# Kernel optimization log

Hardware: AMD Instinct MI355X
Metric: run time of the kernel (lower is better)

## Reference

```python
import jax, jax.numpy as jnp
import numpy as np

N_DRUG, N_CELL, N_EDGES = 10000, 20000, 1280000
D_DRUG, D_CELL, BATCH = 384, 3504, 4096


def setup_inputs() -> dict:
    key = jax.random.key(0)
    ks = jax.random.split(key, 24)
    f32 = jnp.float32

    def lin(kw, kb, fan_in, fan_out, bias=True):
        s = 1.0 / np.sqrt(fan_in)
        W = jax.random.uniform(kw, (fan_in, fan_out), f32, -s, s)
        b = jax.random.uniform(kb, (fan_out,), f32, -s, s) if bias else None
        return W, b

    inp = {}
    inp['drug'] = jax.random.randint(ks[0], (BATCH,), 0, N_DRUG)
    inp['cell'] = jax.random.randint(ks[1], (BATCH,), 0, N_CELL)
    # stored node features / edges (constants in the torch module)
    inp['drug_x'] = jax.random.normal(ks[2], (N_DRUG, D_DRUG), f32)
    inp['cell_x'] = jax.random.normal(ks[3], (N_CELL, D_CELL), f32)
    inp['cell_edges'] = jax.random.randint(ks[4], (2, N_EDGES), 0, N_CELL)
    # drug_emb: Linear(384,128)
    inp['demb_W'], inp['demb_b'] = lin(ks[5], ks[6], D_DRUG, 128)
    # SAGEConv(3504,1024): lin_l (with bias) on aggregated, lin_r (no bias) on root
    inp['c1_lW'], inp['c1_lb'] = lin(ks[7], ks[8], D_CELL, 1024)
    inp['c1_rW'], _ = lin(ks[9], ks[9], D_CELL, 1024, bias=False)
    # SAGEConv(1024,256)
    inp['c2_lW'], inp['c2_lb'] = lin(ks[10], ks[11], 1024, 256)
    inp['c2_rW'], _ = lin(ks[12], ks[12], 1024, 256, bias=False)
    inp['reg_W1'], inp['reg_b1'] = lin(ks[13], ks[14], 384, 384)
    inp['reg_W2'], inp['reg_b2'] = lin(ks[15], ks[16], 384, 384)
    inp['reg_W3'], inp['reg_b3'] = lin(ks[17], ks[18], 384, 1)
    return inp


def _sage(x, src, dst, n, lW, lb, rW):
    # PyG SAGEConv, mean aggregation: lin_l(mean_{j in N(i)} x_j) + lin_r(x_i)
    deg = jax.ops.segment_sum(jnp.ones(src.shape[0], x.dtype), dst, num_segments=n)
    agg = jax.ops.segment_sum(x[src], dst, num_segments=n)  # [n, d_in]
    agg = agg / jnp.maximum(deg, 1.0)[:, None]
    return agg @ lW + lb + x @ rW


def reference(drug, cell, drug_x, cell_x, cell_edges,
              demb_W, demb_b, c1_lW, c1_lb, c1_rW, c2_lW, c2_lb, c2_rW,
              reg_W1, reg_b1, reg_W2, reg_b2, reg_W3, reg_b3):
    src, dst = cell_edges[0], cell_edges[1]
    n = cell_x.shape[0]
    # drug branch: Linear + ReLU (dropout = identity at inference)
    d = jax.nn.relu(drug_x @ demb_W + demb_b)                  # [N_drug, 128]
    # cell branch: two SAGEConv + ReLU
    c = jax.nn.relu(_sage(cell_x, src, dst, n, c1_lW, c1_lb, c1_rW))  # [N_cell, 1024]
    c = jax.nn.relu(_sage(c, src, dst, n, c2_lW, c2_lb, c2_rW))       # [N_cell, 256]
    # gather batch rows and concatenate -> [B, 384]
    x = jnp.concatenate([d[drug], c[cell]], axis=-1)
    x = jax.nn.elu(x @ reg_W1 + reg_b1)
    x = jax.nn.elu(x @ reg_W2 + reg_b2)
    return x @ reg_W3 + reg_b3                                 # [B, 1]
```

## Files before the change

kernel.cpp:

```cpp
#include <hip/hip_runtime.h>
#include <hip/hip_bf16.h>

typedef __bf16 bf16x8 __attribute__((ext_vector_type(8)));
typedef float f32x4 __attribute__((ext_vector_type(4)));
typedef unsigned short u16x8 __attribute__((ext_vector_type(8)));

#define N_DRUG   10000
#define N_CELL   20000
#define NEDGE    1280000
#define D_DRUG   384
#define D_CELL   3504
#define D_CELL_P 3520
#define BATCH    4096

typedef unsigned int u32_g __attribute__((address_space(1)));
typedef unsigned int u32_l __attribute__((address_space(3)));

__device__ __forceinline__ void gld_lds16(const void* g, void* l) {
  __builtin_amdgcn_global_load_lds((const u32_g*)g, (u32_l*)l, 16, 0, 0);
}

__device__ __forceinline__ ushort f2bf(float f) {
  union { float f; unsigned u; } v; v.f = f;
  unsigned r = v.u + 0x7fffu + ((v.u >> 16) & 1u);
  return (ushort)(r >> 16);
}
__device__ __forceinline__ float bf2f(ushort h) {
  union { unsigned u; float f; } v; v.u = ((unsigned)h) << 16;
  return v.f;
}

#define S_BARRIER() asm volatile("s_barrier" ::: "memory")
#define VMCNT6()    asm volatile("s_waitcnt vmcnt(6)" ::: "memory")
#define VMCNT0()    asm volatile("s_waitcnt vmcnt(0)" ::: "memory")


__global__ __launch_bounds__(256) void conv_x(const float* __restrict__ x,
                                              ushort* __restrict__ xb) {
  int idx = blockIdx.x * 256 + threadIdx.x;
  const int CH = D_CELL_P / 8;
  int r = idx / CH, c8 = (idx % CH) * 8;
  if (r >= N_CELL) return;
  ushort4 a, b;
  if (c8 < D_CELL) {
    const float* p = x + (size_t)r * D_CELL + c8;
    float4 v0 = *(const float4*)p;
    float4 v1 = *(const float4*)(p + 4);
    a = make_ushort4(f2bf(v0.x), f2bf(v0.y), f2bf(v0.z), f2bf(v0.w));
    b = make_ushort4(f2bf(v1.x), f2bf(v1.y), f2bf(v1.z), f2bf(v1.w));
  } else {
    a = make_ushort4(0,0,0,0); b = make_ushort4(0,0,0,0);
  }
  ushort* q = xb + (size_t)r * D_CELL_P + c8;
  *(ushort4*)q = a; *(ushort4*)(q + 4) = b;
}

__global__ __launch_bounds__(256) void conv_drug(const float* __restrict__ dx,
                                                 const int* __restrict__ drug,
                                                 ushort* __restrict__ adb) {
  int idx = blockIdx.x * 256 + threadIdx.x;
  int r = idx / 48, c8 = (idx % 48) * 8;
  int g = drug[r];
  const float* p = dx + (size_t)g * D_DRUG + c8;
  float4 v0 = *(const float4*)p, v1 = *(const float4*)(p + 4);
  ushort4 a = make_ushort4(f2bf(v0.x), f2bf(v0.y), f2bf(v0.z), f2bf(v0.w));
  ushort4 b = make_ushort4(f2bf(v1.x), f2bf(v1.y), f2bf(v1.z), f2bf(v1.w));
  ushort* q = adb + (size_t)r * D_DRUG + c8;
  *(ushort4*)q = a; *(ushort4*)(q + 4) = b;
}

__global__ __launch_bounds__(256) void conv_wt(const float* __restrict__ L,
                                               const float* __restrict__ R,
                                               int nL, int N, int Kin, int Kp,
                                               ushort* __restrict__ out) {
  __shared__ float tile[32][33];
  int k0 = blockIdx.x * 32, n0 = blockIdx.y * 32;
  int t = threadIdx.x;
  int tn = t & 31, tk = t >> 5;
  #pragma unroll
  for (int p = 0; p < 4; ++p) {
    int k = k0 + tk + p * 8, n = n0 + tn;
    float v = 0.f;
    if (k < Kin) v = (n < nL) ? L[(size_t)k * nL + n] : R[(size_t)k * (N - nL) + (n - nL)];
    tile[tk + p * 8][tn] = v;
  }
  __syncthreads();
  int wk = t & 31, wn = t >> 5;
  #pragma unroll
  for (int p = 0; p < 4; ++p) {
    int n = n0 + wn + p * 8, k = k0 + wk;
    out[(size_t)n * Kp + k] = f2bf(tile[wk][wn + p * 8]);
  }
}


__global__ void deg_kernel(const int* __restrict__ dst, int* __restrict__ deg, int n) {
  for (int e = blockIdx.x * blockDim.x + threadIdx.x; e < n; e += gridDim.x * blockDim.x)
    atomicAdd(&deg[dst[e]], 1);
}

__global__ __launch_bounds__(1024) void scan_kernel(const int* __restrict__ deg,
                                                    int* __restrict__ rowptr,
                                                    int* __restrict__ cursor, int n) {
  __shared__ int wsum[16];
  __shared__ int carry_s;
  int t = threadIdx.x, wave = t >> 6, lane = t & 63;
  if (t == 0) carry_s = 0;
  __syncthreads();
  for (int base = 0; base < n; base += 1024) {
    int x = (base + t < n) ? deg[base + t] : 0;
    int v = x;
    #pragma unroll
    for (int off = 1; off < 64; off <<= 1) {
      int u = __shfl_up(v, off, 64);
      if (lane >= off) v += u;
    }
    if (lane == 63) wsum[wave] = v;
    __syncthreads();
    if (wave == 0 && lane < 16) {
      int w = wsum[lane];
      #pragma unroll
      for (int off = 1; off < 16; off <<= 1) {
        int u = __shfl_up(w, off, 64);
        if (lane >= off) w += u;
      }
      wsum[lane] = w;
    }
    __syncthreads();
    int wpre = (wave == 0) ? 0 : wsum[wave - 1];
    int incl = v + wpre;
    int carry = carry_s;
    if (base + t < n) { int ex = carry + incl - x; rowptr[base + t] = ex; cursor[base + t] = ex; }
    __syncthreads();
    if (t == 1023) carry_s = carry + incl;
    __syncthreads();
  }
  if (t == 0) rowptr[n] = carry_s;
}

__global__ void bucket_kernel(const int* __restrict__ src, const int* __restrict__ dst,
                              int* __restrict__ cursor, int* __restrict__ srcs, int n) {
  for (int e = blockIdx.x * blockDim.x + threadIdx.x; e < n; e += gridDim.x * blockDim.x) {
    int p = atomicAdd(&cursor[dst[e]], 1);
    srcs[p] = src[e];
  }
}

__global__ void mark_kernel(const int* __restrict__ cell, int* __restrict__ mark) {
  int b = blockIdx.x * 256 + threadIdx.x;
  if (b < BATCH) mark[cell[b]] = 1;
}

__global__ __launch_bounds__(512, 2) void gemm8p(const ushort* __restrict__ A,
                                                 const ushort* __restrict__ Bt,
                                                 float* __restrict__ outF,
                                                 ushort* __restrict__ outB,
                                                 int M) {
  constexpr int K = D_CELL_P;
  constexpr int NK = K / 64;
  __shared__ ushort lds[2][2][32][512];

  const int t = threadIdx.x;
  const int wid = t >> 6, lane = t & 63;
  const int wr = wid >> 2, wc = wid & 3;
  const int brow = blockIdx.y * 256, bcol = blockIdx.x * 256;
  const int fr = lane & 15, kgi = lane >> 4;
  const int slot8 = (fr * 4 + (kgi ^ ((fr >> 1) & 3))) * 8;
  const int srow = lane >> 2;
  const int gsw = ((lane & 3) ^ ((lane >> 3) & 3)) * 8;

  f32x4 acc[8][4];
  #pragma unroll
  for (int m = 0; m < 8; ++m)
    #pragma unroll
    for (int n = 0; n < 4; ++n) acc[m][n] = f32x4{0.f, 0.f, 0.f, 0.f};

  bf16x8 af[4][2], bfg[4][2];

  auto stage = [&](int b, int h, int kt) {
    const ushort* base = (h < 2) ? A : Bt;
    const int rb = (h < 2) ? brow : bcol;
    const int half = h & 1, ab = h >> 1;
    const int k0 = kt * 64;
    #pragma unroll
    for (int j = 0; j < 2; ++j) {
      int c = j * 8 + wid;
      int r16 = half * 8 + (c >> 1), kc = c & 1;
      int row = rb + r16 * 16 + srow;
      if (h < 2) row = row < M ? row : M - 1;
      gld_lds16(base + (size_t)row * K + k0 + kc * 32 + gsw,
                &lds[b][ab][half * 16 + c][0]);
    }
  };

  stage(0, 0, 0); stage(0, 2, 0); stage(0, 3, 0); stage(0, 1, 0);
  stage(1, 0, 1); stage(1, 2, 1); stage(1, 3, 1);
  VMCNT6();
  S_BARRIER();

  for (int kt = 0; kt < NK; ++kt) {
    const int b = kt & 1, nb = b ^ 1;
    const bool dr = (kt >= NK - 2);

    #pragma unroll
    for (int m = 0; m < 4; ++m) {
      af[m][0] = *(const bf16x8*)&lds[b][0][(2 * m + wr) * 2 + 0][slot8];
      af[m][1] = *(const bf16x8*)&lds[b][0][(2 * m + wr) * 2 + 1][slot8];
    }
    #pragma unroll
    for (int n = 0; n < 2; ++n) {
      bfg[n][0] = *(const bf16x8*)&lds[b][1][(4 * n + wc) * 2 + 0][slot8];
      bfg[n][1] = *(const bf16x8*)&lds[b][1][(4 * n + wc) * 2 + 1][slot8];
    }
    if (kt + 1 < NK) stage(nb, 1, kt + 1);
    S_BARRIER();
    __builtin_amdgcn_s_setprio(1);
    #pragma unroll
    for (int m = 0; m < 4; ++m)
      #pragma unroll
      for (int n = 0; n < 2; ++n) {
        acc[m][n] = __builtin_amdgcn_mfma_f32_16x16x32_bf16(af[m][0], bfg[n][0], acc[m][n], 0, 0, 0);
        acc[m][n] = __builtin_amdgcn_mfma_f32_16x16x32_bf16(af[m][1], bfg[n][1], acc[m][n], 0, 0, 0);
      }
    __builtin_amdgcn_s_setprio(0);
    S_BARRIER();

    #pragma unroll
    for (int n = 2; n < 4; ++n) {
      bfg[n][0] = *(const bf16x8*)&lds[b][1][(4 * n + wc) * 2 + 0][slot8];
      bfg[n][1] = *(const bf16x8*)&lds[b][1][(4 * n + wc) * 2 + 1][slot8];
    }
    if (kt + 2 < NK) stage(b, 0, kt + 2);
    S_BARRIER();
    __builtin_amdgcn_s_setprio(1);
    #pragma unroll
    for (int m = 0; m < 4; ++m)
      #pragma unroll
      for (int n = 2; n < 4; ++n) {
        acc[m][n] = __builtin_amdgcn_mfma_f32_16x16x32_bf16(af[m][0], bfg[n][0], acc[m][n], 0, 0, 0);
        acc[m][n] = __builtin_amdgcn_mfma_f32_16x16x32_bf16(af[m][1], bfg[n][1], acc[m][n], 0, 0, 0);
      }
    __builtin_amdgcn_s_setprio(0);
    S_BARRIER();

    #pragma unroll
    for (int m = 0; m < 4; ++m) {
      af[m][0] = *(const bf16x8*)&lds[b][0][(2 * (m + 4) + wr) * 2 + 0][slot8];
      af[m][1] = *(const bf16x8*)&lds[b][0][(2 * (m + 4) + wr) * 2 + 1][slot8];
    }
    if (kt + 2 < NK) stage(b, 2, kt + 2);
    S_BARRIER();
    __builtin_amdgcn_s_setprio(1);
    #pragma unroll
    for (int m = 0; m < 4; ++m)
      #pragma unroll
      for (int n = 0; n < 2; ++n) {
        acc[m + 4][n] = __builtin_amdgcn_mfma_f32_16x16x32_bf16(af[m][0], bfg[n][0], acc[m + 4][n], 0, 0, 0);
        acc[m + 4][n] = __builtin_amdgcn_mfma_f32_16x16x32_bf16(af[m][1], bfg[n][1], acc[m + 4][n], 0, 0, 0);
      }
    __builtin_amdgcn_s_setprio(0);
    S_BARRIER();

    if (kt + 2 < NK) stage(b, 3, kt + 2);
    S_BARRIER();
    __builtin_amdgcn_s_setprio(1);
    #pragma unroll
    for (int m = 0; m < 4; ++m)
      #pragma unroll
      for (int n = 2; n < 4; ++n) {
        acc[m + 4][n] = __builtin_amdgcn_mfma_f32_16x16x32_bf16(af[m][0], bfg[n][0], acc[m + 4][n], 0, 0, 0);
        acc[m + 4][n] = __builtin_amdgcn_mfma_f32_16x16x32_bf16(af[m][1], bfg[n][1], acc[m + 4][n], 0, 0, 0);
      }
    __builtin_amdgcn_s_setprio(0);
    if (dr) { VMCNT0(); } else { VMCNT6(); }
    S_BARRIER();
  }

  #pragma unroll
  for (int m = 0; m < 8; ++m)
    #pragma unroll
    for (int n = 0; n < 4; ++n)
      #pragma unroll
      for (int j = 0; j < 4; ++j) {
        int row = brow + (2 * m + wr) * 16 + kgi * 4 + j;
        int col = bcol + (4 * n + wc) * 16 + fr;
        if (row < M) {
          float v = acc[m][n][j];
          if (col < 1024) outB[(size_t)row * 1024 + col] = f2bf(v);
          else            outF[(size_t)row * 1024 + (col - 1024)] = v;
        }
      }
}

template <int EPI>
__global__ __launch_bounds__(256) void gemm_bt(const ushort* __restrict__ A,
                                               const ushort* __restrict__ Bt,
                                               float* __restrict__ outF,
                                               ushort* __restrict__ outB,
                                               const float* __restrict__ bias,
                                               int M, int N, int K, int ldc) {
  __shared__ ushort ldsA[128 * 32];
  __shared__ ushort ldsB[128 * 32];
  const int t = threadIdx.x;
  const int wave = t >> 6, lane = t & 63;
  const int brow = blockIdx.y * 128;
  const int bcol = blockIdx.x * 128;
  const int wr = wave >> 1, wc = wave & 1;

  f32x4 acc[4][4];
  #pragma unroll
  for (int m = 0; m < 4; ++m)
    #pragma unroll
    for (int n = 0; n < 4; ++n) acc[m][n] = f32x4{0.f, 0.f, 0.f, 0.f};

  const int srow = lane >> 2;
  const int gsw  = ((lane & 3) ^ ((lane >> 3) & 3)) * 8;
  const int nk = K >> 5;

  const int fr = lane & 15;
  const int kgi = lane >> 4;
  const int slot = (fr * 4 + (kgi ^ ((fr >> 1) & 3))) * 8;

  for (int kt = 0; kt < nk; ++kt) {
    const int k0 = kt * 32;
    #pragma unroll
    for (int i = 0; i < 2; ++i) {
      int c = i * 4 + wave;
      int arow = brow + c * 16 + srow;
      arow = arow < M ? arow : M - 1;
      gld_lds16(A + (size_t)arow * K + k0 + gsw, ldsA + c * 512);
      int brB = bcol + c * 16 + srow;
      gld_lds16(Bt + (size_t)brB * K + k0 + gsw, ldsB + c * 512);
    }
    __syncthreads();
    bf16x8 af[4], bf[4];
    #pragma unroll
    for (int m = 0; m < 4; ++m) af[m] = *(const bf16x8*)(ldsA + (wr * 4 + m) * 512 + slot);
    #pragma unroll
    for (int n = 0; n < 4; ++n) bf[n] = *(const bf16x8*)(ldsB + (wc * 4 + n) * 512 + slot);
    #pragma unroll
    for (int m = 0; m < 4; ++m)
      #pragma unroll
      for (int n = 0; n < 4; ++n)
        acc[m][n] = __builtin_amdgcn_mfma_f32_16x16x32_bf16(af[m], bf[n], acc[m][n], 0, 0, 0);
    __syncthreads();
  }

  const int fq = lane >> 4;
  #pragma unroll
  for (int m = 0; m < 4; ++m) {
    #pragma unroll
    for (int n = 0; n < 4; ++n) {
      #pragma unroll
      for (int j = 0; j < 4; ++j) {
        int row = brow + wr * 64 + m * 16 + fq * 4 + j;
        int col = bcol + wc * 64 + n * 16 + fr;
        if (row < M) {
          float v = acc[m][n][j];
          if constexpr (EPI == 0) {
            outF[(size_t)row * ldc + col] = v;
          } else if constexpr (EPI == 2) {
            v += bias[col];
            v = fmaxf(v, 0.f);
            outB[(size_t)row * ldc + col] = f2bf(v);
          } else {
            v += bias[col];
            v = v > 0.f ? v : expm1f(v);
            outB[(size_t)row * ldc + col] = f2bf(v);
          }
        }
      }
    }
  }
}


__global__ __launch_bounds__(256) void agg1_c1(const ushort* __restrict__ Ylb,
                                               const float* __restrict__ Yr,
                                               const float* __restrict__ lb,
                                               const int* __restrict__ rowptr,
                                               const int* __restrict__ srcs,
                                               ushort* __restrict__ c1b) {
  const int b = blockIdx.x, t = threadIdx.x;
  const int s = b & 7;
  const int i = (b >> 3) * 4 + (t >> 6);
  const int lane = t & 63;
  const int eg = lane >> 4, c16 = lane & 15;
  const int s0 = rowptr[i], s1 = rowptr[i + 1];
  const ushort* base = Ylb + s * 128 + c16 * 8;

  float a[8] = {0.f, 0.f, 0.f, 0.f, 0.f, 0.f, 0.f, 0.f};
  int e = s0 + eg;
  for (; e + 4 < s1; e += 8) {
    int srcA = srcs[e], srcB = srcs[e + 4];
    u16x8 vA = *(const u16x8*)(base + (size_t)srcA * 1024);
    u16x8 vB = *(const u16x8*)(base + (size_t)srcB * 1024);
    #pragma unroll
    for (int k = 0; k < 8; ++k) a[k] += bf2f(vA[k]) + bf2f(vB[k]);
  }
  for (; e < s1; e += 4) {
    int src = srcs[e];
    u16x8 v = *(const u16x8*)(base + (size_t)src * 1024);
    #pragma unroll
    for (int k = 0; k < 8; ++k) a[k] += bf2f(v[k]);
  }
  #pragma unroll
  for (int k = 0; k < 8; ++k) {
    a[k] += __shfl_xor(a[k], 16, 64);
    a[k] += __shfl_xor(a[k], 32, 64);
  }
  if (eg == 0) {
    float inv = 1.0f / fmaxf((float)(s1 - s0), 1.0f);
    size_t off = (size_t)i * 1024 + s * 128 + c16 * 8;
    float4 y0 = *(const float4*)(Yr + off);
    float4 y1 = *(const float4*)(Yr + off + 4);
    float yr[8] = {y0.x, y0.y, y0.z, y0.w, y1.x, y1.y, y1.z, y1.w};
    u16x8 o;
    #pragma unroll
    for (int k = 0; k < 8; ++k) {
      float v = a[k] * inv + lb[s * 128 + c16 * 8 + k] + yr[k];
      o[k] = f2bf(fmaxf(v, 0.f));
    }
    *(u16x8*)(c1b + off) = o;
  }
}

__global__ __launch_bounds__(256) void agg2_c2(const float* __restrict__ Z,
                                               const float* __restrict__ lb,
                                               const int* __restrict__ rowptr,
                                               const int* __restrict__ srcs,
                                               const int* __restrict__ mark,
                                               ushort* __restrict__ c2v) {
  int i = blockIdx.x;
  if (!mark[i]) return;
  __shared__ int sl[256];
  int t = threadIdx.x;
  int s0 = rowptr[i], s1 = rowptr[i + 1];
  float a = 0.f;
  for (int base = s0; base < s1; base += 256) {
    int m = s1 - base; if (m > 256) m = 256;
    if (t < m) sl[t] = srcs[base + t];
    __syncthreads();
    int e = 0;
    for (; e + 4 <= m; e += 4) {
      float zA = Z[(size_t)sl[e] * 512 + t];
      float zB = Z[(size_t)sl[e + 1] * 512 + t];
      float zC = Z[(size_t)sl[e + 2] * 512 + t];
      float zD = Z[(size_t)sl[e + 3] * 512 + t];
      a += zA + zB + zC + zD;
    }
    for (; e < m; ++e) a += Z[(size_t)sl[e] * 512 + t];
    __syncthreads();
  }
  float inv = 1.0f / fmaxf((float)(s1 - s0), 1.0f);
  float v = a * inv + lb[t] + Z[(size_t)i * 512 + 256 + t];
  c2v[(size_t)i * 256 + t] = f2bf(fmaxf(v, 0.f));
}

__global__ __launch_bounds__(256) void xcat2(const ushort* __restrict__ c2v,
                                             const int* __restrict__ cell,
                                             ushort* __restrict__ xcat) {
  int idx = blockIdx.x * 256 + threadIdx.x;
  int b = idx >> 6, q = idx & 63;
  ushort4 v = *(const ushort4*)(c2v + (size_t)cell[b] * 256 + q * 4);
  *(ushort4*)(xcat + (size_t)b * 384 + 128 + q * 4) = v;
}

__global__ __launch_bounds__(256) void final_k(const ushort* __restrict__ h2,
                                               const float* __restrict__ W3,
                                               const float* __restrict__ b3,
                                               float* __restrict__ out) {
  int row = blockIdx.x * 4 + (threadIdx.x >> 6);
  int lane = threadIdx.x & 63;
  const ushort* p = h2 + (size_t)row * 384;
  float s = 0.f;
  #pragma unroll
  for (int k = lane; k < 384; k += 64) s += bf2f(p[k]) * W3[k];
  #pragma unroll
  for (int off = 32; off; off >>= 1) s += __shfl_xor(s, off, 64);
  if (lane == 0) out[row] = s + b3[0];
}


extern "C" void kernel_launch(void* const* d_in, const int* in_sizes, int n_in,
                              void* d_out, int out_size, void* d_ws, size_t ws_size,
                              hipStream_t stream) {
  (void)in_sizes; (void)n_in; (void)out_size; (void)ws_size;
  const int*   drug   = (const int*)  d_in[0];
  const int*   cell   = (const int*)  d_in[1];
  const float* drug_x = (const float*)d_in[2];
  const float* cell_x = (const float*)d_in[3];
  const int*   edges  = (const int*)  d_in[4];
  const float* demb_W = (const float*)d_in[5];
  const float* demb_b = (const float*)d_in[6];
  const float* c1_lW  = (const float*)d_in[7];
  const float* c1_lb  = (const float*)d_in[8];
  const float* c1_rW  = (const float*)d_in[9];
  const float* c2_lW  = (const float*)d_in[10];
  const float* c2_lb  = (const float*)d_in[11];
  const float* c2_rW  = (const float*)d_in[12];
  const float* reg_W1 = (const float*)d_in[13];
  const float* reg_b1 = (const float*)d_in[14];
  const float* reg_W2 = (const float*)d_in[15];
  const float* reg_b2 = (const float*)d_in[16];
  const float* reg_W3 = (const float*)d_in[17];
  const float* reg_b3 = (const float*)d_in[18];
  float* out = (float*)d_out;

  char* ws = (char*)d_ws;
  size_t off = 0;
  auto alloc = [&](size_t b) { size_t o = off; off += (b + 255) & ~(size_t)255; return o; };
  size_t oXB  = alloc((size_t)N_CELL * D_CELL_P * 2);
  size_t oW1T = alloc((size_t)2048 * D_CELL_P * 2);
  size_t oYLB = alloc((size_t)N_CELL * 1024 * 2);
  size_t oYR  = alloc((size_t)N_CELL * 1024 * 4);
  size_t oW2T = alloc((size_t)512 * 1024 * 2);
  size_t oSRC = alloc((size_t)NEDGE * 4);
  size_t oDEG = alloc((size_t)N_CELL * 4);
  size_t oRPT = alloc((size_t)(N_CELL + 1) * 4);
  size_t oCUR = alloc((size_t)N_CELL * 4);
  size_t oMRK = alloc((size_t)N_CELL * 4);
  size_t oADB = alloc((size_t)BATCH * D_DRUG * 2);
  size_t oWDT = alloc((size_t)128 * 384 * 2);
  size_t oXC  = alloc((size_t)BATCH * 384 * 2);
  size_t oW1R = alloc((size_t)384 * 384 * 2);
  size_t oW2R = alloc((size_t)384 * 384 * 2);
  size_t oH1  = alloc((size_t)BATCH * 384 * 2);
  size_t oH2  = alloc((size_t)BATCH * 384 * 2);

  ushort* Xb   = (ushort*)(ws + oXB);
  ushort* c1b  = (ushort*)(ws + oXB);
  float*  Z    = (float*) (ws + oXB + 40960000);
  ushort* c2v  = (ushort*)(ws + oXB + 81920000);
  ushort* W1t  = (ushort*)(ws + oW1T);
  ushort* Ylb  = (ushort*)(ws + oYLB);
  float*  Yr   = (float*) (ws + oYR);
  ushort* W2t  = (ushort*)(ws + oW2T);
  int*    srcs = (int*)   (ws + oSRC);
  int*    deg  = (int*)   (ws + oDEG);
  int*    rpt  = (int*)   (ws + oRPT);
  int*    cur  = (int*)   (ws + oCUR);
  int*    mrk  = (int*)   (ws + oMRK);
  ushort* Adb  = (ushort*)(ws + oADB);
  ushort* Wdt  = (ushort*)(ws + oWDT);
  ushort* xcat = (ushort*)(ws + oXC);
  ushort* W1rt = (ushort*)(ws + oW1R);
  ushort* W2rt = (ushort*)(ws + oW2R);
  ushort* h1   = (ushort*)(ws + oH1);
  ushort* h2   = (ushort*)(ws + oH2);

  const int* esrc = edges;
  const int* edst = edges + NEDGE;

  hipMemsetAsync(deg, 0, (size_t)N_CELL * 4, stream);
  hipMemsetAsync(mrk, 0, (size_t)N_CELL * 4, stream);

  deg_kernel<<<2048, 256, 0, stream>>>(edst, deg, NEDGE);
  scan_kernel<<<1, 1024, 0, stream>>>(deg, rpt, cur, N_CELL);
  bucket_kernel<<<2048, 256, 0, stream>>>(esrc, edst, cur, srcs, NEDGE);
  mark_kernel<<<BATCH / 256, 256, 0, stream>>>(cell, mrk);

  conv_x<<<(N_CELL * (D_CELL_P / 8)) / 256, 256, 0, stream>>>(cell_x, Xb);
  conv_wt<<<dim3(D_CELL_P / 32, 2048 / 32), 256, 0, stream>>>(c1_lW, c1_rW, 1024, 2048, D_CELL, D_CELL_P, W1t);
  conv_wt<<<dim3(1024 / 32, 512 / 32), 256, 0, stream>>>(c2_lW, c2_rW, 256, 512, 1024, 1024, W2t);
  conv_wt<<<dim3(384 / 32, 128 / 32), 256, 0, stream>>>(demb_W, demb_W, 128, 128, 384, 384, Wdt);
  conv_wt<<<dim3(384 / 32, 384 / 32), 256, 0, stream>>>(reg_W1, reg_W1, 384, 384, 384, 384, W1rt);
  conv_wt<<<dim3(384 / 32, 384 / 32), 256, 0, stream>>>(reg_W2, reg_W2, 384, 384, 384, 384, W2rt);
  conv_drug<<<(BATCH * (D_DRUG / 8)) / 256, 256, 0, stream>>>(drug_x, drug, Adb);

  gemm8p<<<dim3(2048 / 256, (N_CELL + 255) / 256), 512, 0, stream>>>(
      Xb, W1t, Yr, Ylb, N_CELL);
  agg1_c1<<<(N_CELL / 4) * 8, 256, 0, stream>>>(Ylb, Yr, c1_lb, rpt, srcs, c1b);

  gemm_bt<0><<<dim3(512 / 128, (N_CELL + 127) / 128), 256, 0, stream>>>(
      c1b, W2t, Z, nullptr, nullptr, N_CELL, 512, 1024, 512);
  agg2_c2<<<N_CELL, 256, 0, stream>>>(Z, c2_lb, rpt, srcs, mrk, c2v);

  gemm_bt<2><<<dim3(1, BATCH / 128), 256, 0, stream>>>(
      Adb, Wdt, nullptr, xcat, demb_b, BATCH, 128, 384, 384);
  xcat2<<<(BATCH * 64) / 256, 256, 0, stream>>>(c2v, cell, xcat);

  gemm_bt<3><<<dim3(384 / 128, BATCH / 128), 256, 0, stream>>>(
      xcat, W1rt, nullptr, h1, reg_b1, BATCH, 384, 384, 384);
  gemm_bt<3><<<dim3(384 / 128, BATCH / 128), 256, 0, stream>>>(
      h1, W2rt, nullptr, h2, reg_b2, BATCH, 384, 384, 384);
  final_k<<<BATCH / 4, 256, 0, stream>>>(h2, reg_W3, reg_b3, out);
}
```

Baseline: 903.9 us.

## Restructure GEMM main loop into two k-halves with whole-tile prefetch

```diff
diff --git a/kernel.cpp b/kernel.cpp
--- a/kernel.cpp
+++ b/kernel.cpp
@@ -31,7 +31,8 @@
 }
 
 #define S_BARRIER() asm volatile("s_barrier" ::: "memory")
-#define VMCNT6()    asm volatile("s_waitcnt vmcnt(6)" ::: "memory")
+#define LGKMCNT0()  asm volatile("s_waitcnt lgkmcnt(0)" ::: "memory")
+#define VMCNT8()    asm volatile("s_waitcnt vmcnt(8)" ::: "memory")
 #define VMCNT0()    asm volatile("s_waitcnt vmcnt(0)" ::: "memory")
 
 
@@ -175,8 +176,6 @@
     #pragma unroll
     for (int n = 0; n < 4; ++n) acc[m][n] = f32x4{0.f, 0.f, 0.f, 0.f};
 
-  bf16x8 af[4][2], bfg[4][2];
-
   auto stage = [&](int b, int h, int kt) {
     const ushort* base = (h < 2) ? A : Bt;
     const int rb = (h < 2) ? brow : bcol;
@@ -193,87 +192,56 @@
     }
   };
 
-  stage(0, 0, 0); stage(0, 2, 0); stage(0, 3, 0); stage(0, 1, 0);
-  stage(1, 0, 1); stage(1, 2, 1); stage(1, 3, 1);
-  VMCNT6();
+  stage(0, 0, 0); stage(0, 1, 0); stage(0, 2, 0); stage(0, 3, 0);
+  stage(1, 0, 1); stage(1, 1, 1); stage(1, 2, 1); stage(1, 3, 1);
+  VMCNT8();
   S_BARRIER();
 
   for (int kt = 0; kt < NK; ++kt) {
-    const int b = kt & 1, nb = b ^ 1;
-    const bool dr = (kt >= NK - 2);
-
-    #pragma unroll
-    for (int m = 0; m < 4; ++m) {
-      af[m][0] = *(const bf16x8*)&lds[b][0][(2 * m + wr) * 2 + 0][slot8];
-      af[m][1] = *(const bf16x8*)&lds[b][0][(2 * m + wr) * 2 + 1][slot8];
-    }
-    #pragma unroll
-    for (int n = 0; n < 2; ++n) {
-      bfg[n][0] = *(const bf16x8*)&lds[b][1][(4 * n + wc) * 2 + 0][slot8];
-      bfg[n][1] = *(const bf16x8*)&lds[b][1][(4 * n + wc) * 2 + 1][slot8];
-    }
-    if (kt + 1 < NK) stage(nb, 1, kt + 1);
-    S_BARRIER();
-    __builtin_amdgcn_s_setprio(1);
-    #pragma unroll
-    for (int m = 0; m < 4; ++m)
-      #pragma unroll
-      for (int n = 0; n < 2; ++n) {
-        acc[m][n] = __builtin_amdgcn_mfma_f32_16x16x32_bf16(af[m][0], bfg[n][0], acc[m][n], 0, 0, 0);
-        acc[m][n] = __builtin_amdgcn_mfma_f32_16x16x32_bf16(af[m][1], bfg[n][1], acc[m][n], 0, 0, 0);
+    const int b = kt & 1;
+    const bool last2 = (kt + 2 >= NK);
+
+    {
+      bf16x8 a0[8], b0[4];
+      #pragma unroll
+      for (int m = 0; m < 8; ++m)
+        a0[m] = *(const bf16x8*)&lds[b][0][(2 * m + wr) * 2 + 0][slot8];
+      #pragma unroll
+      for (int n = 0; n < 4; ++n)
+        b0[n] = *(const bf16x8*)&lds[b][1][(4 * n + wc) * 2 + 0][slot8];
+      __builtin_amdgcn_s_setprio(1);
+      #pragma unroll
+      for (int m = 0; m < 8; ++m)
+        #pragma unroll
+        for (int n = 0; n < 4; ++n)
+          acc[m][n] = __builtin_amdgcn_mfma_f32_16x16x32_bf16(a0[m], b0[n], acc[m][n], 0, 0, 0);
+      __builtin_amdgcn_s_setprio(0);
+    }
+
+    {
+      bf16x8 a1[8], b1[4];
+      #pragma unroll
+      for (int m = 0; m < 8; ++m)
+        a1[m] = *(const bf16x8*)&lds[b][0][(2 * m + wr) * 2 + 1][slot8];
+      #pragma unroll
+      for (int n = 0; n < 4; ++n)
+        b1[n] = *(const bf16x8*)&lds[b][1][(4 * n + wc) * 2 + 1][slot8];
+      LGKMCNT0();
+      S_BARRIER();
+      if (!last2) {
+        stage(b, 0, kt + 2); stage(b, 1, kt + 2);
+        stage(b, 2, kt + 2); stage(b, 3, kt + 2);
       }
-    __builtin_amdgcn_s_setprio(0);
-    S_BARRIER();
-
-    #pragma unroll
-    for (int n = 2; n < 4; ++n) {
-      bfg[n][0] = *(const bf16x8*)&lds[b][1][(4 * n + wc) * 2 + 0][slot8];
-      bfg[n][1] = *(const bf16x8*)&lds[b][1][(4 * n + wc) * 2 + 1][slot8];
-    }
-    if (kt + 2 < NK) stage(b, 0, kt + 2);
-    S_BARRIER();
-    __builtin_amdgcn_s_setprio(1);
-    #pragma unroll
-    for (int m = 0; m < 4; ++m)
-      #pragma unroll
-      for (int n = 2; n < 4; ++n) {
-        acc[m][n] = __builtin_amdgcn_mfma_f32_16x16x32_bf16(af[m][0], bfg[n][0], acc[m][n], 0, 0, 0);
-        acc[m][n] = __builtin_amdgcn_mfma_f32_16x16x32_bf16(af[m][1], bfg[n][1], acc[m][n], 0, 0, 0);
-      }
-    __builtin_amdgcn_s_setprio(0);
-    S_BARRIER();
-
-    #pragma unroll
-    for (int m = 0; m < 4; ++m) {
-      af[m][0] = *(const bf16x8*)&lds[b][0][(2 * (m + 4) + wr) * 2 + 0][slot8];
-      af[m][1] = *(const bf16x8*)&lds[b][0][(2 * (m + 4) + wr) * 2 + 1][slot8];
-    }
-    if (kt + 2 < NK) stage(b, 2, kt + 2);
-    S_BARRIER();
-    __builtin_amdgcn_s_setprio(1);
-    #pragma unroll
-    for (int m = 0; m < 4; ++m)
-      #pragma unroll
-      for (int n = 0; n < 2; ++n) {
-        acc[m + 4][n] = __builtin_amdgcn_mfma_f32_16x16x32_bf16(af[m][0], bfg[n][0], acc[m + 4][n], 0, 0, 0);
-        acc[m + 4][n] = __builtin_amdgcn_mfma_f32_16x16x32_bf16(af[m][1], bfg[n][1], acc[m + 4][n], 0, 0, 0);
-      }
-    __builtin_amdgcn_s_setprio(0);
-    S_BARRIER();
-
-    if (kt + 2 < NK) stage(b, 3, kt + 2);
-    S_BARRIER();
-    __builtin_amdgcn_s_setprio(1);
-    #pragma unroll
-    for (int m = 0; m < 4; ++m)
-      #pragma unroll
-      for (int n = 2; n < 4; ++n) {
-        acc[m + 4][n] = __builtin_amdgcn_mfma_f32_16x16x32_bf16(af[m][0], bfg[n][0], acc[m + 4][n], 0, 0, 0);
-        acc[m + 4][n] = __builtin_amdgcn_mfma_f32_16x16x32_bf16(af[m][1], bfg[n][1], acc[m + 4][n], 0, 0, 0);
-      }
-    __builtin_amdgcn_s_setprio(0);
-    if (dr) { VMCNT0(); } else { VMCNT6(); }
-    S_BARRIER();
+      __builtin_amdgcn_s_setprio(1);
+      #pragma unroll
+      for (int m = 0; m < 8; ++m)
+        #pragma unroll
+        for (int n = 0; n < 4; ++n)
+          acc[m][n] = __builtin_amdgcn_mfma_f32_16x16x32_bf16(a1[m], b1[n], acc[m][n], 0, 0, 0);
+      __builtin_amdgcn_s_setprio(0);
+      if (last2) { VMCNT0(); } else { VMCNT8(); }
+      S_BARRIER();
+    }
   }
 
   #pragma unroll
```

Result: slower. 938.9 us (+3.9%).

## Switch big GEMM to 32x32x16 MFMA tiles with reorganized staging

Applied to the files above, without the earlier changes.

```diff
diff --git a/kernel.cpp b/kernel.cpp
--- a/kernel.cpp
+++ b/kernel.cpp
@@ -3,6 +3,7 @@
 
 typedef __bf16 bf16x8 __attribute__((ext_vector_type(8)));
 typedef float f32x4 __attribute__((ext_vector_type(4)));
+typedef float f32x16 __attribute__((ext_vector_type(16)));
 typedef unsigned short u16x8 __attribute__((ext_vector_type(8)));
 
 #define N_DRUG   10000
@@ -31,7 +32,7 @@
 }
 
 #define S_BARRIER() asm volatile("s_barrier" ::: "memory")
-#define VMCNT6()    asm volatile("s_waitcnt vmcnt(6)" ::: "memory")
+#define VMCNT4()    asm volatile("s_waitcnt vmcnt(4)" ::: "memory")
 #define VMCNT0()    asm volatile("s_waitcnt vmcnt(0)" ::: "memory")
 
 
@@ -164,128 +165,131 @@
   const int wid = t >> 6, lane = t & 63;
   const int wr = wid >> 2, wc = wid & 3;
   const int brow = blockIdx.y * 256, bcol = blockIdx.x * 256;
-  const int fr = lane & 15, kgi = lane >> 4;
-  const int slot8 = (fr * 4 + (kgi ^ ((fr >> 1) & 3))) * 8;
   const int srow = lane >> 2;
   const int gsw = ((lane & 3) ^ ((lane >> 3) & 3)) * 8;
-
-  f32x4 acc[8][4];
-  #pragma unroll
-  for (int m = 0; m < 8; ++m)
-    #pragma unroll
-    for (int n = 0; n < 4; ++n) acc[m][n] = f32x4{0.f, 0.f, 0.f, 0.f};
-
-  bf16x8 af[4][2], bfg[4][2];
-
-  auto stage = [&](int b, int h, int kt) {
-    const ushort* base = (h < 2) ? A : Bt;
-    const int rb = (h < 2) ? brow : bcol;
-    const int half = h & 1, ab = h >> 1;
-    const int k0 = kt * 64;
+  const int rl = lane & 31, h = lane >> 5;
+  const int fr = rl & 15, rbit = rl >> 4;
+
+  f32x16 acc[4][2];
+  #pragma unroll
+  for (int m = 0; m < 4; ++m)
+    #pragma unroll
+    for (int n = 0; n < 2; ++n)
+      #pragma unroll
+      for (int r = 0; r < 16; ++r) acc[m][n][r] = 0.f;
+
+  auto ldA = [&](int b, int tm, int s) -> bf16x8 {
+    int r16 = wr * 8 + tm * 2 + rbit;
+    int ch = r16 * 2 + (s >> 1);
+    int g = (s & 1) * 2 + h;
+    return *(const bf16x8*)&lds[b][0][ch][(fr * 4 + (g ^ ((fr >> 1) & 3))) * 8];
+  };
+  auto ldB = [&](int b, int tn, int s) -> bf16x8 {
+    int r16 = wc * 4 + tn * 2 + rbit;
+    int ch = r16 * 2 + (s >> 1);
+    int g = (s & 1) * 2 + h;
+    return *(const bf16x8*)&lds[b][1][ch][(fr * 4 + (g ^ ((fr >> 1) & 3))) * 8];
+  };
+  auto stageA = [&](int b, int mg, int kt) {
     #pragma unroll
     for (int j = 0; j < 2; ++j) {
-      int c = j * 8 + wid;
-      int r16 = half * 8 + (c >> 1), kc = c & 1;
-      int row = rb + r16 * 16 + srow;
-      if (h < 2) row = row < M ? row : M - 1;
-      gld_lds16(base + (size_t)row * K + k0 + kc * 32 + gsw,
-                &lds[b][ab][half * 16 + c][0]);
+      int idx = j * 8 + wid;
+      int wrq = idx >> 3, tm2 = (idx >> 2) & 1, bit = (idx >> 1) & 1, kc = idx & 1;
+      int r16 = wrq * 8 + mg * 4 + tm2 * 2 + bit;
+      int row = brow + r16 * 16 + srow;
+      row = row < M ? row : M - 1;
+      gld_lds16(A + (size_t)row * K + kt * 64 + kc * 32 + gsw, &lds[b][0][r16 * 2 + kc][0]);
     }
   };
-
-  stage(0, 0, 0); stage(0, 2, 0); stage(0, 3, 0); stage(0, 1, 0);
-  stage(1, 0, 1); stage(1, 2, 1); stage(1, 3, 1);
-  VMCNT6();
+  auto stageB = [&](int b, int tn, int kt) {
+    #pragma unroll
+    for (int j = 0; j < 2; ++j) {
+      int idx = j * 8 + wid;
+      int wcq = idx >> 2, bit = (idx >> 1) & 1, kc = idx & 1;
+      int r16 = wcq * 4 + tn * 2 + bit;
+      int row = bcol + r16 * 16 + srow;
+      gld_lds16(Bt + (size_t)row * K + kt * 64 + kc * 32 + gsw, &lds[b][1][r16 * 2 + kc][0]);
+    }
+  };
+
+  stageA(0, 0, 0); stageB(0, 0, 0); stageA(0, 1, 0); stageB(0, 1, 0);
+  stageA(1, 0, 1); stageB(1, 0, 1);
+  VMCNT4();
   S_BARRIER();
 
   for (int kt = 0; kt < NK; ++kt) {
     const int b = kt & 1, nb = b ^ 1;
-    const bool dr = (kt >= NK - 2);
-
-    #pragma unroll
-    for (int m = 0; m < 4; ++m) {
-      af[m][0] = *(const bf16x8*)&lds[b][0][(2 * m + wr) * 2 + 0][slot8];
-      af[m][1] = *(const bf16x8*)&lds[b][0][(2 * m + wr) * 2 + 1][slot8];
-    }
-    #pragma unroll
-    for (int n = 0; n < 2; ++n) {
-      bfg[n][0] = *(const bf16x8*)&lds[b][1][(4 * n + wc) * 2 + 0][slot8];
-      bfg[n][1] = *(const bf16x8*)&lds[b][1][(4 * n + wc) * 2 + 1][slot8];
-    }
-    if (kt + 1 < NK) stage(nb, 1, kt + 1);
+    const bool last2 = (kt + 2 >= NK);
+    bf16x8 a01[2][4], a23[2][4], b0[4], b1[4];
+
+    #pragma unroll
+    for (int tm = 0; tm < 2; ++tm)
+      #pragma unroll
+      for (int s = 0; s < 4; ++s) a01[tm][s] = ldA(b, tm, s);
+    #pragma unroll
+    for (int s = 0; s < 4; ++s) b0[s] = ldB(b, 0, s);
+    if (kt + 1 < NK) stageA(nb, 1, kt + 1);
     S_BARRIER();
     __builtin_amdgcn_s_setprio(1);
     #pragma unroll
-    for (int m = 0; m < 4; ++m)
-      #pragma unroll
-      for (int n = 0; n < 2; ++n) {
-        acc[m][n] = __builtin_amdgcn_mfma_f32_16x16x32_bf16(af[m][0], bfg[n][0], acc[m][n], 0, 0, 0);
-        acc[m][n] = __builtin_amdgcn_mfma_f32_16x16x32_bf16(af[m][1], bfg[n][1], acc[m][n], 0, 0, 0);
-      }
+    for (int tm = 0; tm < 2; ++tm)
+      #pragma unroll
+      for (int s = 0; s < 4; ++s)
+        acc[tm][0] = __builtin_amdgcn_mfma_f32_32x32x16_bf16(a01[tm][s], b0[s], acc[tm][0], 0, 0, 0);
     __builtin_amdgcn_s_setprio(0);
     S_BARRIER();
 
     #pragma unroll
-    for (int n = 2; n < 4; ++n) {
-      bfg[n][0] = *(const bf16x8*)&lds[b][1][(4 * n + wc) * 2 + 0][slot8];
-      bfg[n][1] = *(const bf16x8*)&lds[b][1][(4 * n + wc) * 2 + 1][slot8];
-    }
-    if (kt + 2 < NK) stage(b, 0, kt + 2);
+    for (int tm = 0; tm < 2; ++tm)
+      #pragma unroll
+      for (int s = 0; s < 4; ++s) a23[tm][s] = ldA(b, tm + 2, s);
+    if (kt + 1 < NK) stageB(nb, 1, kt + 1);
     S_BARRIER();
     __builtin_amdgcn_s_setprio(1);
     #pragma unroll
-    for (int m = 0; m < 4; ++m)
-      #pragma unroll
-      for (int n = 2; n < 4; ++n) {
-        acc[m][n] = __builtin_amdgcn_mfma_f32_16x16x32_bf16(af[m][0], bfg[n][0], acc[m][n], 0, 0, 0);
-        acc[m][n] = __builtin_amdgcn_mfma_f32_16x16x32_bf16(af[m][1], bfg[n][1], acc[m][n], 0, 0, 0);
-      }
+    for (int tm = 0; tm < 2; ++tm)
+      #pragma unroll
+      for (int s = 0; s < 4; ++s)
+        acc[tm + 2][0] = __builtin_amdgcn_mfma_f32_32x32x16_bf16(a23[tm][s], b0[s], acc[tm + 2][0], 0, 0, 0);
     __builtin_amdgcn_s_setprio(0);
     S_BARRIER();
 
     #pragma unroll
-    for (int m = 0; m < 4; ++m) {
-      af[m][0] = *(const bf16x8*)&lds[b][0][(2 * (m + 4) + wr) * 2 + 0][slot8];
-      af[m][1] = *(const bf16x8*)&lds[b][0][(2 * (m + 4) + wr) * 2 + 1][slot8];
-    }
-    if (kt + 2 < NK) stage(b, 2, kt + 2);
+    for (int s = 0; s < 4; ++s) b1[s] = ldB(b, 1, s);
+    if (kt + 2 < NK) stageB(b, 0, kt + 2);
     S_BARRIER();
     __builtin_amdgcn_s_setprio(1);
     #pragma unroll
-    for (int m = 0; m < 4; ++m)
-      #pragma unroll
-      for (int n = 0; n < 2; ++n) {
-        acc[m + 4][n] = __builtin_amdgcn_mfma_f32_16x16x32_bf16(af[m][0], bfg[n][0], acc[m + 4][n], 0, 0, 0);
-        acc[m + 4][n] = __builtin_amdgcn_mfma_f32_16x16x32_bf16(af[m][1], bfg[n][1], acc[m + 4][n], 0, 0, 0);
-      }
+    for (int tm = 0; tm < 2; ++tm)
+      #pragma unroll
+      for (int s = 0; s < 4; ++s)
+        acc[tm + 2][1] = __builtin_amdgcn_mfma_f32_32x32x16_bf16(a23[tm][s], b1[s], acc[tm + 2][1], 0, 0, 0);
     __builtin_amdgcn_s_setprio(0);
     S_BARRIER();
 
-    if (kt + 2 < NK) stage(b, 3, kt + 2);
+    if (kt + 2 < NK) stageA(b, 0, kt + 2);
     S_BARRIER();
     __builtin_amdgcn_s_setprio(1);
     #pragma unroll
-    for (int m = 0; m < 4; ++m)
-      #pragma unroll
-      for (int n = 2; n < 4; ++n) {
-        acc[m + 4][n] = __builtin_amdgcn_mfma_f32_16x16x32_bf16(af[m][0], bfg[n][0], acc[m + 4][n], 0, 0, 0);
-        acc[m + 4][n] = __builtin_amdgcn_mfma_f32_16x16x32_bf16(af[m][1], bfg[n][1], acc[m + 4][n], 0, 0, 0);
-      }
+    for (int tm = 0; tm < 2; ++tm)
+      #pragma unroll
+      for (int s = 0; s < 4; ++s)
+        acc[tm][1] = __builtin_amdgcn_mfma_f32_32x32x16_bf16(a01[tm][s], b1[s], acc[tm][1], 0, 0, 0);
     __builtin_amdgcn_s_setprio(0);
-    if (dr) { VMCNT0(); } else { VMCNT6(); }
-    S_BARRIER();
-  }
-
-  #pragma unroll
-  for (int m = 0; m < 8; ++m)
-    #pragma unroll
-    for (int n = 0; n < 4; ++n)
-      #pragma unroll
-      for (int j = 0; j < 4; ++j) {
-        int row = brow + (2 * m + wr) * 16 + kgi * 4 + j;
-        int col = bcol + (4 * n + wc) * 16 + fr;
+    if (last2) { VMCNT0(); } else { VMCNT4(); }
+    S_BARRIER();
+  }
+
+  #pragma unroll
+  for (int tm = 0; tm < 4; ++tm)
+    #pragma unroll
+    for (int tn = 0; tn < 2; ++tn)
+      #pragma unroll
+      for (int r = 0; r < 16; ++r) {
+        int row = brow + wr * 128 + tm * 32 + (r & 3) + 8 * (r >> 2) + 4 * h;
+        int col = bcol + wc * 64 + tn * 32 + rl;
         if (row < M) {
-          float v = acc[m][n][j];
+          float v = acc[tm][tn][r];
           if (col < 1024) outB[(size_t)row * 1024 + col] = f2bf(v);
           else            outF[(size_t)row * 1024 + (col - 1024)] = v;
         }
```

Result: slower. 966.4 us (+6.9%).

## Reuse 256x256 GEMM for conv2 with bf16 output and vectorized bf16 aggregation

Applied to the files above, without the earlier changes.

```diff
diff --git a/kernel.cpp b/kernel.cpp
--- a/kernel.cpp
+++ b/kernel.cpp
@@ -151,13 +151,13 @@
   if (b < BATCH) mark[cell[b]] = 1;
 }
 
+template <int EPI>
 __global__ __launch_bounds__(512, 2) void gemm8p(const ushort* __restrict__ A,
                                                  const ushort* __restrict__ Bt,
                                                  float* __restrict__ outF,
                                                  ushort* __restrict__ outB,
-                                                 int M) {
-  constexpr int K = D_CELL_P;
-  constexpr int NK = K / 64;
+                                                 int M, int K) {
+  const int NK = K / 64;
   __shared__ ushort lds[2][2][32][512];
 
   const int t = threadIdx.x;
@@ -286,8 +286,12 @@
         int col = bcol + (4 * n + wc) * 16 + fr;
         if (row < M) {
           float v = acc[m][n][j];
-          if (col < 1024) outB[(size_t)row * 1024 + col] = f2bf(v);
-          else            outF[(size_t)row * 1024 + (col - 1024)] = v;
+          if constexpr (EPI == 0) {
+            if (col < 1024) outB[(size_t)row * 1024 + col] = f2bf(v);
+            else            outF[(size_t)row * 1024 + (col - 1024)] = v;
+          } else {
+            outB[(size_t)row * 512 + col] = f2bf(v);
+          }
         }
       }
 }
@@ -425,7 +429,7 @@
   }
 }
 
-__global__ __launch_bounds__(256) void agg2_c2(const float* __restrict__ Z,
+__global__ __launch_bounds__(256) void agg2_c2(const ushort* __restrict__ Zb,
                                                const float* __restrict__ lb,
                                                const int* __restrict__ rowptr,
                                                const int* __restrict__ srcs,
@@ -433,28 +437,45 @@
                                                ushort* __restrict__ c2v) {
   int i = blockIdx.x;
   if (!mark[i]) return;
-  __shared__ int sl[256];
+  __shared__ float red[4][32][8];
   int t = threadIdx.x;
+  int sub = t >> 5, c = t & 31;
+  int wave = t >> 6, lane = t & 63;
   int s0 = rowptr[i], s1 = rowptr[i + 1];
-  float a = 0.f;
-  for (int base = s0; base < s1; base += 256) {
-    int m = s1 - base; if (m > 256) m = 256;
-    if (t < m) sl[t] = srcs[base + t];
-    __syncthreads();
-    int e = 0;
-    for (; e + 4 <= m; e += 4) {
-      float zA = Z[(size_t)sl[e] * 512 + t];
-      float zB = Z[(size_t)sl[e + 1] * 512 + t];
-      float zC = Z[(size_t)sl[e + 2] * 512 + t];
-      float zD = Z[(size_t)sl[e + 3] * 512 + t];
-      a += zA + zB + zC + zD;
-    }
-    for (; e < m; ++e) a += Z[(size_t)sl[e] * 512 + t];
-    __syncthreads();
-  }
-  float inv = 1.0f / fmaxf((float)(s1 - s0), 1.0f);
-  float v = a * inv + lb[t] + Z[(size_t)i * 512 + 256 + t];
-  c2v[(size_t)i * 256 + t] = f2bf(fmaxf(v, 0.f));
+  float a[8] = {0.f, 0.f, 0.f, 0.f, 0.f, 0.f, 0.f, 0.f};
+  int e = s0 + sub;
+  for (; e + 8 < s1; e += 16) {
+    int sA = srcs[e], sB = srcs[e + 8];
+    u16x8 vA = *(const u16x8*)(Zb + (size_t)sA * 512 + c * 8);
+    u16x8 vB = *(const u16x8*)(Zb + (size_t)sB * 512 + c * 8);
+    #pragma unroll
+    for (int k = 0; k < 8; ++k) a[k] += bf2f(vA[k]) + bf2f(vB[k]);
+  }
+  for (; e < s1; e += 8) {
+    int src = srcs[e];
+    u16x8 v = *(const u16x8*)(Zb + (size_t)src * 512 + c * 8);
+    #pragma unroll
+    for (int k = 0; k < 8; ++k) a[k] += bf2f(v[k]);
+  }
+  #pragma unroll
+  for (int k = 0; k < 8; ++k) a[k] += __shfl_xor(a[k], 32, 64);
+  if (lane < 32) {
+    #pragma unroll
+    for (int k = 0; k < 8; ++k) red[wave][lane][k] = a[k];
+  }
+  __syncthreads();
+  if (t < 32) {
+    float inv = 1.0f / fmaxf((float)(s1 - s0), 1.0f);
+    u16x8 r = *(const u16x8*)(Zb + (size_t)i * 512 + 256 + t * 8);
+    u16x8 o;
+    #pragma unroll
+    for (int k = 0; k < 8; ++k) {
+      float sum = red[0][t][k] + red[1][t][k] + red[2][t][k] + red[3][t][k];
+      float v = sum * inv + lb[t * 8 + k] + bf2f(r[k]);
+      o[k] = f2bf(fmaxf(v, 0.f));
+    }
+    *(u16x8*)(c2v + (size_t)i * 256 + t * 8) = o;
+  }
 }
 
 __global__ __launch_bounds__(256) void xcat2(const ushort* __restrict__ c2v,
@@ -530,7 +551,7 @@
 
   ushort* Xb   = (ushort*)(ws + oXB);
   ushort* c1b  = (ushort*)(ws + oXB);
-  float*  Z    = (float*) (ws + oXB + 40960000);
+  ushort* Zb   = (ushort*)(ws + oXB + 40960000);
   ushort* c2v  = (ushort*)(ws + oXB + 81920000);
   ushort* W1t  = (ushort*)(ws + oW1T);
   ushort* Ylb  = (ushort*)(ws + oYLB);
@@ -568,13 +589,13 @@
   conv_wt<<<dim3(384 / 32, 384 / 32), 256, 0, stream>>>(reg_W2, reg_W2, 384, 384, 384, 384, W2rt);
   conv_drug<<<(BATCH * (D_DRUG / 8)) / 256, 256, 0, stream>>>(drug_x, drug, Adb);
 
-  gemm8p<<<dim3(2048 / 256, (N_CELL + 255) / 256), 512, 0, stream>>>(
-      Xb, W1t, Yr, Ylb, N_CELL);
+  gemm8p<0><<<dim3(2048 / 256, (N_CELL + 255) / 256), 512, 0, stream>>>(
+      Xb, W1t, Yr, Ylb, N_CELL, D_CELL_P);
   agg1_c1<<<(N_CELL / 4) * 8, 256, 0, stream>>>(Ylb, Yr, c1_lb, rpt, srcs, c1b);
 
-  gemm_bt<0><<<dim3(512 / 128, (N_CELL + 127) / 128), 256, 0, stream>>>(
-      c1b, W2t, Z, nullptr, nullptr, N_CELL, 512, 1024, 512);
-  agg2_c2<<<N_CELL, 256, 0, stream>>>(Z, c2_lb, rpt, srcs, mrk, c2v);
+  gemm8p<1><<<dim3(512 / 256, (N_CELL + 255) / 256), 512, 0, stream>>>(
+      c1b, W2t, nullptr, Zb, N_CELL, 1024);
+  agg2_c2<<<N_CELL, 256, 0, stream>>>(Zb, c2_lb, rpt, srcs, mrk, c2v);
 
   gemm_bt<2><<<dim3(1, BATCH / 128), 256, 0, stream>>>(
       Adb, Wdt, nullptr, xcat, demb_b, BATCH, 128, 384, 384);
```

Result: slower. 935.0 us (+3.4%).
